# Optimization experiments

Hardware: AMD Instinct MI355X
Metric: run time of the kernel (lower is better)

The kernel has to match this reference:

```python
import jax, jax.numpy as jnp
import numpy as np

H = 512      # hidden_size
Z = 128      # z_dim
E = 512      # embedding_dim
D = 2 * H + Z  # GRU hidden / decoder state dim = 1152
V = 32000    # output_size
BS = 256
N = 128      # encoder nodes per source


def setup_inputs() -> dict:
    key = jax.random.key(0)
    ks = jax.random.split(key, 24)
    s = 0.05
    inp = {
        "prev_y": jax.random.normal(ks[0], (BS, E), jnp.float32),
        "prev_h": jax.random.normal(ks[1], (BS, D), jnp.float32),
        "equ_enc": jax.random.normal(ks[2], (BS, N, H), jnp.float32),
        "sns_enc": jax.random.normal(ks[3], (BS, N, H), jnp.float32),
        "z_sample": jax.random.normal(ks[4], (BS, Z), jnp.float32),
        "equ_mask": jax.random.randint(ks[5], (BS, N), 0, 2) > 0,
        "sns_mask": jax.random.randint(ks[6], (BS, N), 0, 2) > 0,
        # Attention (equ): W1: HxH, W2: HxD, vt: 1xH (torch Linear weight = [out,in])
        "W1e": jax.random.normal(ks[7], (H, H), jnp.float32) * s,
        "W2e": jax.random.normal(ks[8], (H, D), jnp.float32) * s,
        "vte": jax.random.normal(ks[9], (1, H), jnp.float32) * s,
        "W1s": jax.random.normal(ks[10], (H, H), jnp.float32) * s,
        "W2s": jax.random.normal(ks[11], (H, D), jnp.float32) * s,
        "vts": jax.random.normal(ks[12], (1, H), jnp.float32) * s,
        "plan_W": jax.random.normal(ks[13], (2, D), jnp.float32) * s,
        "plan_b": jax.random.normal(ks[14], (2,), jnp.float32) * s,
        "Wc": jax.random.normal(ks[15], (H, E + H), jnp.float32) * s,
        "bc": jax.random.normal(ks[16], (H,), jnp.float32) * s,
        # GRU: input H -> hidden D
        "w_ih": jax.random.normal(ks[17], (3 * D, H), jnp.float32) * s,
        "w_hh": jax.random.normal(ks[18], (3 * D, D), jnp.float32) * s,
        "b_ih": jax.random.normal(ks[19], (3 * D,), jnp.float32) * s,
        "b_hh": jax.random.normal(ks[20], (3 * D,), jnp.float32) * s,
        "Wout": jax.random.normal(ks[21], (V, D), jnp.float32) * s,
        "bout": jax.random.normal(ks[22], (V,), jnp.float32) * s,
    }
    return inp


def _attn(h, enc, mask, W1, W2, vt):
    # enc: (b,n,H), h: (b,D)
    et = jnp.einsum('bnh,kh->bnk', enc, W1)          # (b,n,H)
    dt = (h @ W2.T)[:, None, :]                       # (b,1,H)
    u = jnp.einsum('bnh,h->bn', jnp.tanh(et + dt), vt[0])
    u = jnp.where(mask, -jnp.inf, u)
    return jax.nn.softmax(u, axis=-1)                 # (b,n)


def reference(prev_y, prev_h, equ_enc, sns_enc, z_sample, equ_mask, sns_mask,
              W1e, W2e, vte, W1s, W2s, vts, plan_W, plan_b, Wc, bc,
              w_ih, w_hh, b_ih, b_hh, Wout, bout):
    aw_e = _attn(prev_h, equ_enc, equ_mask, W1e, W2e, vte)
    ctx_e = jnp.einsum('bn,bnh->bh', aw_e, equ_enc)
    aw_s = _attn(prev_h, sns_enc, sns_mask, W1s, W2s, vts)
    ctx_s = jnp.einsum('bn,bnh->bh', aw_s, sns_enc)
    plan = jax.nn.softmax(prev_h @ plan_W.T + plan_b, axis=-1)  # (b,2)
    combine = jnp.stack([ctx_e, ctx_s], axis=1)                  # (b,2,H)
    context = jnp.einsum('bk,bkh->bh', plan, combine)
    y_ctx = jnp.concatenate([prev_y, context], axis=-1)          # (b,E+H)
    x = y_ctx @ Wc.T + bc                                        # (b,H)
    # single-step GRU (torch gate order: r, z, n)
    gx = x @ w_ih.T + b_ih                                       # (b,3D)
    gh = prev_h @ w_hh.T + b_hh
    Dh = prev_h.shape[-1]
    gx_r, gx_z, gx_n = gx[:, :Dh], gx[:, Dh:2*Dh], gx[:, 2*Dh:]
    gh_r, gh_z, gh_n = gh[:, :Dh], gh[:, Dh:2*Dh], gh[:, 2*Dh:]
    r = jax.nn.sigmoid(gx_r + gh_r)
    zg = jax.nn.sigmoid(gx_z + gh_z)
    n = jnp.tanh(gx_n + r * gh_n)
    h_new = (1.0 - zg) * n + zg * prev_h                          # (b,D)
    dec_output = (h_new @ Wout.T + bout)[:, None, :]              # (b,1,V)
    dec_hidden = h_new[None]                                      # (1,b,D)
    return dec_output, dec_hidden, plan
```

## Files before the change

### kernel.cpp

```cpp
#include <hip/hip_runtime.h>
#include <stdint.h>
#include <math.h>

#define BS_  256
#define NSEQ 128
#define HH   512
#define DD   1152
#define VV   32000
#define BN_  (BS_*NSEQ)

typedef float  f32x4  __attribute__((ext_vector_type(4)));
typedef __bf16 bf16x8 __attribute__((ext_vector_type(8)));

__device__ __forceinline__ f32x4 mfma16(bf16x8 a, bf16x8 b, f32x4 c) {
    return __builtin_amdgcn_mfma_f32_16x16x32_bf16(a, b, c, 0, 0, 0);
}

__device__ __forceinline__ bf16x8 pack8(f32x4 a, f32x4 b) {
    bf16x8 v;
    v[0] = (__bf16)a[0]; v[1] = (__bf16)a[1]; v[2] = (__bf16)a[2]; v[3] = (__bf16)a[3];
    v[4] = (__bf16)b[0]; v[5] = (__bf16)b[1]; v[6] = (__bf16)b[2]; v[7] = (__bf16)b[3];
    return v;
}

__device__ __forceinline__ float tanh_fast(float x) {
    float e = __expf(2.f * x);
    return 1.f - __fdividef(2.f, e + 1.f);
}

__device__ __forceinline__ void gload16(const void* g, void* l) {
    __builtin_amdgcn_global_load_lds(
        (const __attribute__((address_space(1))) void*)g,
        (__attribute__((address_space(3))) void*)l, 16, 0, 0);
}

__global__ __launch_bounds__(256) void k_cast(const float* __restrict__ src,
                                              __bf16* __restrict__ dst, int n8)
{
    int i = blockIdx.x * 256 + threadIdx.x;
    int stride = gridDim.x * 256;
    for (; i < n8; i += stride) {
        const f32x4* s = (const f32x4*)(src + (size_t)i * 8);
        f32x4 a = s[0], b = s[1];
        *(bf16x8*)(dst + (size_t)i * 8) = pack8(a, b);
    }
}

__global__ __launch_bounds__(256) void k_attn2(
    const float* __restrict__ enc_e, const float* __restrict__ enc_s,
    const __bf16* __restrict__ W1be, const __bf16* __restrict__ W1bs,
    const float* __restrict__ vte, const float* __restrict__ vts,
    const float* __restrict__ dt_e, const float* __restrict__ dt_s,
    float* __restrict__ u_part)
{
    const int L = blockIdx.x;
    const int n = (L >> 3) & 3;
    const int G = (L & 7) + ((L >> 5) << 3);
    const int e = G >> 8;
    const int b = G & 255;

    const float*  enc = e ? enc_s : enc_e;
    const __bf16* W1  = e ? W1bs : W1be;
    const float*  vt  = e ? vts : vte;
    const float*  dt  = e ? dt_s : dt_e;

    __shared__ float  lA[2][4096];
    __shared__ __bf16 lB[2][4096];
    __shared__ float  upart[2][128];

    const int t = threadIdx.x;
    const int w = t >> 6, wr = w >> 1, wc = w & 1;
    const int lane = t & 63, g = lane >> 4, r = lane & 15;

    const float*  Ag = enc + (size_t)b * (128 * 512);
    const __bf16* Bg = W1 + (size_t)n * (128 * 512);

    int aoff[4], boff[2], aldsb[4], bldsb[2];
    #pragma unroll
    for (int i = 0; i < 4; ++i) {
        int c = i * 256 + w * 64 + lane;
        int row = c >> 3, kc = c & 7;
        aoff[i]  = row * 512 + ((kc ^ (row & 7)) << 2);
        aldsb[i] = (i * 256 + w * 64) << 2;
    }
    #pragma unroll
    for (int i = 0; i < 2; ++i) {
        int c = i * 256 + w * 64 + lane;
        int row = c >> 2, kc = c & 3;
        boff[i]  = row * 512 + ((kc ^ ((row >> 1) & 3)) << 3);
        bldsb[i] = (i * 256 + w * 64) << 3;
    }

    f32x4 acc[4][4];
    #pragma unroll
    for (int i = 0; i < 4; ++i)
        #pragma unroll
        for (int j = 0; j < 4; ++j) acc[i][j] = (f32x4){0.f, 0.f, 0.f, 0.f};

    #pragma unroll
    for (int i = 0; i < 4; ++i) gload16(Ag + aoff[i], &lA[0][aldsb[i]]);
    #pragma unroll
    for (int i = 0; i < 2; ++i) gload16(Bg + boff[i], &lB[0][bldsb[i]]);

    for (int kb = 0; kb < 16; ++kb) {
        const int buf = kb & 1;
        __syncthreads();
        if (kb + 1 < 16) {
            const int k0 = (kb + 1) * 32;
            #pragma unroll
            for (int i = 0; i < 4; ++i) gload16(Ag + aoff[i] + k0, &lA[buf ^ 1][aldsb[i]]);
            #pragma unroll
            for (int i = 0; i < 2; ++i) gload16(Bg + boff[i] + k0, &lB[buf ^ 1][bldsb[i]]);
        }
        bf16x8 af[4], bfr[4];
        #pragma unroll
        for (int j = 0; j < 4; ++j) {
            int row = wc * 64 + j * 16 + r;
            bfr[j] = *(const bf16x8*)&lB[buf][row * 32 + ((g ^ ((row >> 1) & 3)) << 3)];
        }
        #pragma unroll
        for (int i = 0; i < 4; ++i) {
            int row = wr * 64 + i * 16 + r;
            int s = row & 7;
            f32x4 a0 = *(const f32x4*)&lA[buf][row * 32 + (((g << 1) ^ s) << 2)];
            f32x4 a1 = *(const f32x4*)&lA[buf][row * 32 + ((((g << 1) | 1) ^ s) << 2)];
            af[i] = pack8(a0, a1);
        }
        #pragma unroll
        for (int i = 0; i < 4; ++i)
            #pragma unroll
            for (int j = 0; j < 4; ++j)
                acc[i][j] = mfma16(af[i], bfr[j], acc[i][j]);
    }

    float dv[4], vv[4];
    #pragma unroll
    for (int j = 0; j < 4; ++j) {
        int col = n * 128 + wc * 64 + j * 16 + r;
        dv[j] = dt[(size_t)b * 512 + col];
        vv[j] = vt[col];
    }
    #pragma unroll
    for (int i = 0; i < 4; ++i) {
        #pragma unroll
        for (int q = 0; q < 4; ++q) {
            float s = 0.f;
            #pragma unroll
            for (int j = 0; j < 4; ++j)
                s += vv[j] * tanh_fast(acc[i][j][q] + dv[j]);
            #pragma unroll
            for (int m = 1; m < 16; m <<= 1) s += __shfl_xor(s, m);
            if (r == 0) upart[wc][wr * 64 + i * 16 + g * 4 + q] = s;
        }
    }
    __syncthreads();
    if (t < 128)
        u_part[((size_t)(n * 2 + e)) * BN_ + b * 128 + t] = upart[0][t] + upart[1][t];
}

__global__ __launch_bounds__(256) void k_vocab2(
    const __bf16* __restrict__ A,
    const float* __restrict__ B,
    const float* __restrict__ bias, float* __restrict__ C)
{
    const int L = blockIdx.x;
    const int p  = (L & 7) + ((L >> 4) << 3);
    const int rr = (L >> 3) & 1;
    if (p >= 250) return;
    const int rb = rr * 128, cb = p * 128;

    __shared__ __bf16 lA[2][4096];
    __shared__ float  lB[2][4096];

    const int t = threadIdx.x;
    const int w = t >> 6, wr = w >> 1, wc = w & 1;
    const int lane = t & 63, g = lane >> 4, r = lane & 15;

    const __bf16* Ag = A + (size_t)rb * DD;
    const float*  Bg = B + (size_t)cb * DD;

    int aoff[2], boff[4], aldsb[2], bldsb[4];
    #pragma unroll
    for (int i = 0; i < 2; ++i) {
        int c = i * 256 + w * 64 + lane;
        int row = c >> 2, kc = c & 3;
        aoff[i]  = row * DD + ((kc ^ ((row >> 1) & 3)) << 3);
        aldsb[i] = (i * 256 + w * 64) << 3;
    }
    #pragma unroll
    for (int i = 0; i < 4; ++i) {
        int c = i * 256 + w * 64 + lane;
        int row = c >> 3, kc = c & 7;
        boff[i]  = row * DD + ((kc ^ (row & 7)) << 2);
        bldsb[i] = (i * 256 + w * 64) << 2;
    }

    f32x4 acc[4][4];
    #pragma unroll
    for (int i = 0; i < 4; ++i)
        #pragma unroll
        for (int j = 0; j < 4; ++j) acc[i][j] = (f32x4){0.f, 0.f, 0.f, 0.f};

    #pragma unroll
    for (int i = 0; i < 2; ++i) gload16(Ag + aoff[i], &lA[0][aldsb[i]]);
    #pragma unroll
    for (int i = 0; i < 4; ++i) gload16(Bg + boff[i], &lB[0][bldsb[i]]);

    for (int kb = 0; kb < 36; ++kb) {
        const int buf = kb & 1;
        __syncthreads();
        if (kb + 1 < 36) {
            const int k0 = (kb + 1) * 32;
            #pragma unroll
            for (int i = 0; i < 2; ++i) gload16(Ag + aoff[i] + k0, &lA[buf ^ 1][aldsb[i]]);
            #pragma unroll
            for (int i = 0; i < 4; ++i) gload16(Bg + boff[i] + k0, &lB[buf ^ 1][bldsb[i]]);
        }
        bf16x8 af[4], bfr[4];
        #pragma unroll
        for (int i = 0; i < 4; ++i) {
            int row = wr * 64 + i * 16 + r;
            af[i] = *(const bf16x8*)&lA[buf][row * 32 + ((g ^ ((row >> 1) & 3)) << 3)];
        }
        #pragma unroll
        for (int j = 0; j < 4; ++j) {
            int row = wc * 64 + j * 16 + r;
            int s = row & 7;
            f32x4 b0 = *(const f32x4*)&lB[buf][row * 32 + (((g << 1) ^ s) << 2)];
            f32x4 b1 = *(const f32x4*)&lB[buf][row * 32 + ((((g << 1) | 1) ^ s) << 2)];
            bfr[j] = pack8(b0, b1);
        }
        #pragma unroll
        for (int i = 0; i < 4; ++i)
            #pragma unroll
            for (int j = 0; j < 4; ++j)
                acc[i][j] = mfma16(af[i], bfr[j], acc[i][j]);
    }

    #pragma unroll
    for (int j = 0; j < 4; ++j) {
        const int col = cb + wc * 64 + j * 16 + r;
        const float bv = bias[col];
        #pragma unroll
        for (int i = 0; i < 4; ++i) {
            #pragma unroll
            for (int q = 0; q < 4; ++q) {
                const int row = rb + wr * 64 + i * 16 + g * 4 + q;
                C[(size_t)row * VV + col] = acc[i][j][q] + bv;
            }
        }
    }
}

__global__ __launch_bounds__(256) void k_tile128(
    const float* __restrict__ A, const float* __restrict__ B,
    const float* __restrict__ bias, float* __restrict__ C,
    int K, int ldc)
{
    const int rb = blockIdx.x * 128;
    const int cb = blockIdx.y * 128;
    const int t = threadIdx.x;
    const int w = t >> 6, wr = w >> 1, wc = w & 1;
    const int lane = t & 63, g = lane >> 4, r = lane & 15;
    const int s_row = t >> 1, s_h = t & 1;

    __shared__ bf16x8 sm[2][2][512];

    const float* Ap = A + (size_t)(rb + s_row) * K + s_h * 16;
    const float* Bp = B + (size_t)(cb + s_row) * K + s_h * 16;

    const int kg0 = 2 * s_h, kg1 = 2 * s_h + 1;
    const int swz0 = kg0 * 128 + ((s_row & 112) | ((s_row ^ (kg0 << 2)) & 15));
    const int swz1 = kg1 * 128 + ((s_row & 112) | ((s_row ^ (kg1 << 2)) & 15));

    int ai[4], bi[4];
    #pragma unroll
    for (int i = 0; i < 4; ++i) {
        ai[i] = g * 128 + wr * 64 + i * 16 + ((r ^ (g << 2)) & 15);
        bi[i] = g * 128 + wc * 64 + i * 16 + ((r ^ (g << 2)) & 15);
    }

    const int KS = K >> 5;
    f32x4 pa0 = ((const f32x4*)Ap)[0], pa1 = ((const f32x4*)Ap)[1],
          pa2 = ((const f32x4*)Ap)[2], pa3 = ((const f32x4*)Ap)[3];
    f32x4 pb0 = ((const f32x4*)Bp)[0], pb1 = ((const f32x4*)Bp)[1],
          pb2 = ((const f32x4*)Bp)[2], pb3 = ((const f32x4*)Bp)[3];

    f32x4 acc[4][4];
    #pragma unroll
    for (int i = 0; i < 4; ++i)
        #pragma unroll
        for (int j = 0; j < 4; ++j) acc[i][j] = (f32x4){0.f, 0.f, 0.f, 0.f};

    for (int kb = 0; kb < KS; ++kb) {
        const int buf = kb & 1;
        sm[buf][0][swz0] = pack8(pa0, pa1);
        sm[buf][0][swz1] = pack8(pa2, pa3);
        sm[buf][1][swz0] = pack8(pb0, pb1);
        sm[buf][1][swz1] = pack8(pb2, pb3);
        __syncthreads();
        if (kb + 1 < KS) {
            const float* a2 = Ap + (kb + 1) * 32;
            const float* b2 = Bp + (kb + 1) * 32;
            pa0 = ((const f32x4*)a2)[0]; pa1 = ((const f32x4*)a2)[1];
            pa2 = ((const f32x4*)a2)[2]; pa3 = ((const f32x4*)a2)[3];
            pb0 = ((const f32x4*)b2)[0]; pb1 = ((const f32x4*)b2)[1];
            pb2 = ((const f32x4*)b2)[2]; pb3 = ((const f32x4*)b2)[3];
        }
        bf16x8 af[4], bfr[4];
        #pragma unroll
        for (int i = 0; i < 4; ++i) af[i]  = sm[buf][0][ai[i]];
        #pragma unroll
        for (int j = 0; j < 4; ++j) bfr[j] = sm[buf][1][bi[j]];
        #pragma unroll
        for (int i = 0; i < 4; ++i)
            #pragma unroll
            for (int j = 0; j < 4; ++j)
                acc[i][j] = mfma16(af[i], bfr[j], acc[i][j]);
    }

    #pragma unroll
    for (int j = 0; j < 4; ++j) {
        const int col = cb + wc * 64 + j * 16 + r;
        const float bv = bias ? bias[col] : 0.f;
        #pragma unroll
        for (int i = 0; i < 4; ++i) {
            #pragma unroll
            for (int q = 0; q < 4; ++q) {
                const int row = rb + wr * 64 + i * 16 + g * 4 + q;
                C[(size_t)row * ldc + col] = acc[i][j][q] + bv;
            }
        }
    }
}

__global__ __launch_bounds__(256) void k_prevh(
    const float* __restrict__ prev_h, const float* __restrict__ W2e,
    const float* __restrict__ W2s, const float* __restrict__ w_hh,
    const float* __restrict__ b_hh,
    float* __restrict__ dt_e, float* __restrict__ dt_s, float* __restrict__ gh)
{
    const int cb = blockIdx.x * 64;
    const int rb = blockIdx.y * 64;
    const int t  = threadIdx.x;
    const int w = t >> 6, lane = t & 63, g = lane >> 4, r = lane & 15;
    const int s_row = t >> 2, s_kc = t & 3;
    const int K = DD;

    __shared__ bf16x8 sm[2][2][256];

    const float* Ap = prev_h + (size_t)(rb + s_row) * K + s_kc * 8;
    const float* Bp;
    {
        int brow = cb + s_row;
        if (cb < 512)        Bp = W2e + (size_t)brow * K;
        else if (cb < 1024)  Bp = W2s + (size_t)(brow - 512) * K;
        else                 Bp = w_hh + (size_t)(brow - 1024) * K;
        Bp += s_kc * 8;
    }

    const int KS = K >> 5;
    f32x4 pa0 = *(const f32x4*)Ap, pa1 = *(const f32x4*)(Ap + 4);
    f32x4 pb0 = *(const f32x4*)Bp, pb1 = *(const f32x4*)(Bp + 4);

    f32x4 acc[4] = {{0,0,0,0},{0,0,0,0},{0,0,0,0},{0,0,0,0}};

    for (int kb = 0; kb < KS; ++kb) {
        sm[kb & 1][0][s_kc * 64 + s_row] = pack8(pa0, pa1);
        sm[kb & 1][1][s_kc * 64 + s_row] = pack8(pb0, pb1);
        __syncthreads();
        if (kb + 1 < KS) {
            const float* a2 = Ap + (kb + 1) * 32;
            const float* b2 = Bp + (kb + 1) * 32;
            pa0 = *(const f32x4*)a2; pa1 = *(const f32x4*)(a2 + 4);
            pb0 = *(const f32x4*)b2; pb1 = *(const f32x4*)(b2 + 4);
        }
        bf16x8 af = sm[kb & 1][0][g * 64 + w * 16 + r];
        #pragma unroll
        for (int j = 0; j < 4; ++j) {
            bf16x8 bf = sm[kb & 1][1][g * 64 + j * 16 + r];
            acc[j] = mfma16(af, bf, acc[j]);
        }
    }

    #pragma unroll
    for (int j = 0; j < 4; ++j) {
        int col = cb + j * 16 + r;
        #pragma unroll
        for (int q = 0; q < 4; ++q) {
            int row = rb + w * 16 + g * 4 + q;
            float v = acc[j][q];
            if (cb < 512)       dt_e[(size_t)row * 512 + col] = v;
            else if (cb < 1024) dt_s[(size_t)row * 512 + (col - 512)] = v;
            else {
                int c0 = col - 1024;
                gh[(size_t)row * 3456 + c0] = v + b_hh[c0];
            }
        }
    }
}

__global__ __launch_bounds__(256) void k_ctx(
    const float* __restrict__ u_part, const int* __restrict__ mask_e,
    const int* __restrict__ mask_s, const float* __restrict__ enc_e,
    const float* __restrict__ enc_s, const float* __restrict__ prev_h,
    const float* __restrict__ plan_W, const float* __restrict__ plan_b,
    const float* __restrict__ prev_y,
    float* __restrict__ y_ctx, float* __restrict__ plan_out)
{
    const int b = blockIdx.x;
    const int rh = blockIdx.y;
    const int t = threadIdx.x;
    const int lane = t & 63, wid = t >> 6, half = t >> 7, n = t & 127;

    __shared__ float aw[2][128];
    __shared__ float red[16];
    __shared__ float planv[2];

    const int* mask = half ? mask_s : mask_e;
    float uv = u_part[(size_t)(0 * 2 + half) * BN_ + b * 128 + n]
             + u_part[(size_t)(1 * 2 + half) * BN_ + b * 128 + n]
             + u_part[(size_t)(2 * 2 + half) * BN_ + b * 128 + n]
             + u_part[(size_t)(3 * 2 + half) * BN_ + b * 128 + n];
    bool msk = mask[b * 128 + n] != 0;
    float val = msk ? -3.4e38f : uv;

    float mx = val;
    #pragma unroll
    for (int m = 1; m < 64; m <<= 1) mx = fmaxf(mx, __shfl_xor(mx, m));
    if (lane == 0) red[wid] = mx;
    __syncthreads();
    mx = fmaxf(red[half * 2], red[half * 2 + 1]);
    float ex = msk ? 0.f : __expf(uv - mx);
    float sm = ex;
    #pragma unroll
    for (int m = 1; m < 64; m <<= 1) sm += __shfl_xor(sm, m);
    if (lane == 0) red[4 + wid] = sm;
    __syncthreads();
    sm = red[4 + half * 2] + red[4 + half * 2 + 1];
    aw[half][n] = ex / sm;

    float p0 = 0.f, p1 = 0.f;
    for (int i = t; i < DD; i += 256) {
        float hv = prev_h[(size_t)b * DD + i];
        p0 += hv * plan_W[i];
        p1 += hv * plan_W[DD + i];
    }
    #pragma unroll
    for (int m = 1; m < 64; m <<= 1) { p0 += __shfl_xor(p0, m); p1 += __shfl_xor(p1, m); }
    if (lane == 0) { red[8 + wid] = p0; red[12 + wid] = p1; }
    __syncthreads();
    if (t == 0) {
        float l0 = red[8] + red[9] + red[10] + red[11] + plan_b[0];
        float l1 = red[12] + red[13] + red[14] + red[15] + plan_b[1];
        float mm = fmaxf(l0, l1);
        float e0 = __expf(l0 - mm), e1 = __expf(l1 - mm);
        float ss = e0 + e1;
        planv[0] = e0 / ss; planv[1] = e1 / ss;
        if (rh == 0) {
            plan_out[b * 2 + 0] = planv[0];
            plan_out[b * 2 + 1] = planv[1];
        }
    }
    __syncthreads();

    const int ee = t >> 7;
    const int tt = t & 127;
    const float pl = planv[ee];
    const float* base = (ee ? enc_s : enc_e) + (size_t)b * 65536 + (size_t)(rh * 64) * 512 + tt * 4;
    f32x4 accv = {0.f, 0.f, 0.f, 0.f};
    #pragma unroll 4
    for (int row = 0; row < 64; ++row) {
        f32x4 v = *(const f32x4*)(base + (size_t)row * 512);
        float a = aw[ee][rh * 64 + row];
        accv += a * v;
    }
    float* dst = y_ctx + (size_t)b * 1024 + 512 + tt * 4;
    atomicAdd(dst + 0, pl * accv[0]);
    atomicAdd(dst + 1, pl * accv[1]);
    atomicAdd(dst + 2, pl * accv[2]);
    atomicAdd(dst + 3, pl * accv[3]);

    if (rh == 0 && t < 128) {
        f32x4 v = *(const f32x4*)(prev_y + (size_t)b * 512 + t * 4);
        *(f32x4*)(y_ctx + (size_t)b * 1024 + t * 4) = v;
    }
}

__global__ __launch_bounds__(256) void k_gemm_bias(
    const float* __restrict__ A, const float* __restrict__ B,
    const float* __restrict__ bias, float* __restrict__ C,
    int K, int ldc)
{
    const int cb = blockIdx.x * 64;
    const int rb = blockIdx.y * 64;
    const int t  = threadIdx.x;
    const int w = t >> 6, lane = t & 63, g = lane >> 4, r = lane & 15;
    const int s_row = t >> 2, s_kc = t & 3;

    __shared__ bf16x8 sm[2][2][256];

    const float* Ap = A + (size_t)(rb + s_row) * K + s_kc * 8;
    const float* Bp = B + (size_t)(cb + s_row) * K + s_kc * 8;

    const int KS = K >> 5;
    f32x4 pa0 = *(const f32x4*)Ap, pa1 = *(const f32x4*)(Ap + 4);
    f32x4 pb0 = *(const f32x4*)Bp, pb1 = *(const f32x4*)(Bp + 4);

    f32x4 acc[4] = {{0,0,0,0},{0,0,0,0},{0,0,0,0},{0,0,0,0}};

    for (int kb = 0; kb < KS; ++kb) {
        sm[kb & 1][0][s_kc * 64 + s_row] = pack8(pa0, pa1);
        sm[kb & 1][1][s_kc * 64 + s_row] = pack8(pb0, pb1);
        __syncthreads();
        if (kb + 1 < KS) {
            const float* a2 = Ap + (kb + 1) * 32;
            const float* b2 = Bp + (kb + 1) * 32;
            pa0 = *(const f32x4*)a2; pa1 = *(const f32x4*)(a2 + 4);
            pb0 = *(const f32x4*)b2; pb1 = *(const f32x4*)(b2 + 4);
        }
        bf16x8 af = sm[kb & 1][0][g * 64 + w * 16 + r];
        #pragma unroll
        for (int j = 0; j < 4; ++j) {
            bf16x8 bf = sm[kb & 1][1][g * 64 + j * 16 + r];
            acc[j] = mfma16(af, bf, acc[j]);
        }
    }
    #pragma unroll
    for (int j = 0; j < 4; ++j) {
        int col = cb + j * 16 + r;
        float bv = bias ? bias[col] : 0.f;
        #pragma unroll
        for (int q = 0; q < 4; ++q) {
            int row = rb + w * 16 + g * 4 + q;
            C[(size_t)row * ldc + col] = acc[j][q] + bv;
        }
    }
}

__global__ __launch_bounds__(384) void k_gru(
    const float* __restrict__ gx, const float* __restrict__ gh,
    const float* __restrict__ prev_h, float* __restrict__ h_new,
    float* __restrict__ out_hidden, __bf16* __restrict__ h_new_bf)
{
    int d = blockIdx.x * 384 + threadIdx.x;
    int b = blockIdx.y;
    size_t o3 = (size_t)b * 3456;
    float xr = gx[o3 + d], xz = gx[o3 + 1152 + d], xn = gx[o3 + 2304 + d];
    float hr = gh[o3 + d], hz = gh[o3 + 1152 + d], hn = gh[o3 + 2304 + d];
    float rr = 1.f / (1.f + __expf(-(xr + hr)));
    float zz = 1.f / (1.f + __expf(-(xz + hz)));
    float nv = tanhf(xn + rr * hn);
    float hv = (1.f - zz) * nv + zz * prev_h[(size_t)b * DD + d];
    h_new[(size_t)b * DD + d] = hv;
    out_hidden[(size_t)b * DD + d] = hv;
    h_new_bf[(size_t)b * DD + d] = (__bf16)hv;
}

extern "C" void kernel_launch(void* const* d_in, const int* in_sizes, int n_in,
                              void* d_out, int out_size, void* d_ws, size_t ws_size,
                              hipStream_t stream)
{
    const float* prev_y = (const float*)d_in[0];
    const float* prev_h = (const float*)d_in[1];
    const float* enc_e  = (const float*)d_in[2];
    const float* enc_s  = (const float*)d_in[3];
    const int*   mask_e = (const int*)d_in[5];
    const int*   mask_s = (const int*)d_in[6];
    const float* W1e    = (const float*)d_in[7];
    const float* W2e    = (const float*)d_in[8];
    const float* vte    = (const float*)d_in[9];
    const float* W1s    = (const float*)d_in[10];
    const float* W2s    = (const float*)d_in[11];
    const float* vts    = (const float*)d_in[12];
    const float* plan_W = (const float*)d_in[13];
    const float* plan_b = (const float*)d_in[14];
    const float* Wc     = (const float*)d_in[15];
    const float* bc     = (const float*)d_in[16];
    const float* w_ih   = (const float*)d_in[17];
    const float* w_hh   = (const float*)d_in[18];
    const float* b_ih   = (const float*)d_in[19];
    const float* b_hh   = (const float*)d_in[20];
    const float* Wout   = (const float*)d_in[21];
    const float* bout   = (const float*)d_in[22];

    float* out = (float*)d_out;
    float* ws  = (float*)d_ws;

    float* gh     = ws;
    float* big2   = ws + 884736;
    float* upxx   = big2 + 884736;
    float* y_ctx  = upxx + 262144;
    float* h_new  = y_ctx + 262144;
    __bf16* W1be  = (__bf16*)(h_new + 294912);
    __bf16* W1bs  = W1be + 262144;
    __bf16* hnbf  = W1bs + 262144;

    float* dt_e  = big2;
    float* dt_s  = big2 + 131072;
    float* gx    = big2;
    float* u_part = upxx;
    float* xx    = upxx;

    float* dec_out  = out;
    float* dec_hid  = out + 8192000;
    float* plan_out = out + 8486912;

    hipMemsetAsync(y_ctx, 0, 262144 * sizeof(float), stream);

    k_cast<<<dim3(128), 256, 0, stream>>>(W1e, W1be, 32768);
    k_cast<<<dim3(128), 256, 0, stream>>>(W1s, W1bs, 32768);

    k_prevh<<<dim3(70, 4), 256, 0, stream>>>(prev_h, W2e, W2s, w_hh, b_hh,
                                             dt_e, dt_s, gh);

    k_attn2<<<dim3(2048), 256, 0, stream>>>(
        enc_e, enc_s, W1be, W1bs, vte, vts, dt_e, dt_s, u_part);

    k_ctx<<<dim3(BS_, 2), 256, 0, stream>>>(u_part, mask_e, mask_s, enc_e, enc_s,
                                            prev_h, plan_W, plan_b, prev_y,
                                            y_ctx, plan_out);

    k_gemm_bias<<<dim3(8, 4), 256, 0, stream>>>(y_ctx, Wc, bc, xx, 1024, 512);
    k_tile128<<<dim3(2, 27), 256, 0, stream>>>(xx, w_ih, b_ih, gx, 512, 3456);

    k_gru<<<dim3(3, BS_), 384, 0, stream>>>(gx, gh, prev_h, h_new, dec_hid, hnbf);

    k_vocab2<<<dim3(512), 256, 0, stream>>>(hnbf, Wout, bout, dec_out);
}
```

Measured before the change: 579.4 us.

## Fuse attention scoring, softmax and context into one kernel with LDS-resident encoder

Each block now loads one batch row's encoder tile once into shared memory as bf16. It computes scores across all W1 output columns, then the masked softmax and the weighted context sum, all from that resident tile. This removes the repeated fp32 encoder reads from global memory and the separate context kernel. The plan softmax moves to its own small kernel. The trade-off is lower occupancy from the large LDS footprint, plus a context sum computed from bf16-rounded encoder values.

Measured after the change: 582.2 us. About the same (+0.5%).

```diff
diff --git a/kernel.cpp b/kernel.cpp
--- a/kernel.cpp
+++ b/kernel.cpp
@@ -46,116 +46,200 @@
     }
 }
 
-__global__ __launch_bounds__(256) void k_attn2(
+__global__ __launch_bounds__(128) void k_plan(
+    const float* __restrict__ prev_h, const float* __restrict__ plan_W,
+    const float* __restrict__ plan_b, const float* __restrict__ prev_y,
+    float* __restrict__ y_ctx, float* __restrict__ plan_out)
+{
+    const int b = blockIdx.x;
+    const int t = threadIdx.x;
+    const int lane = t & 63, w = t >> 6;
+    __shared__ float red[4];
+
+    float p0 = 0.f, p1 = 0.f;
+    for (int i = t; i < DD; i += 128) {
+        float hv = prev_h[(size_t)b * DD + i];
+        p0 += hv * plan_W[i];
+        p1 += hv * plan_W[DD + i];
+    }
+    #pragma unroll
+    for (int m = 1; m < 64; m <<= 1) { p0 += __shfl_xor(p0, m); p1 += __shfl_xor(p1, m); }
+    if (lane == 0) { red[w] = p0; red[2 + w] = p1; }
+    __syncthreads();
+    if (t == 0) {
+        float l0 = red[0] + red[1] + plan_b[0];
+        float l1 = red[2] + red[3] + plan_b[1];
+        float mm = fmaxf(l0, l1);
+        float e0 = __expf(l0 - mm), e1 = __expf(l1 - mm);
+        float ss = e0 + e1;
+        plan_out[b * 2 + 0] = e0 / ss;
+        plan_out[b * 2 + 1] = e1 / ss;
+    }
+    f32x4 v = *(const f32x4*)(prev_y + (size_t)b * 512 + t * 4);
+    *(f32x4*)(y_ctx + (size_t)b * 1024 + t * 4) = v;
+}
+
+__global__ __launch_bounds__(512, 1) void k_attn3(
     const float* __restrict__ enc_e, const float* __restrict__ enc_s,
     const __bf16* __restrict__ W1be, const __bf16* __restrict__ W1bs,
     const float* __restrict__ vte, const float* __restrict__ vts,
     const float* __restrict__ dt_e, const float* __restrict__ dt_s,
-    float* __restrict__ u_part)
+    const int* __restrict__ mask_e, const int* __restrict__ mask_s,
+    const float* __restrict__ plan_out,
+    float* __restrict__ y_ctx)
 {
     const int L = blockIdx.x;
-    const int n = (L >> 3) & 3;
-    const int G = (L & 7) + ((L >> 5) << 3);
-    const int e = G >> 8;
-    const int b = G & 255;
-
-    const float*  enc = e ? enc_s : enc_e;
-    const __bf16* W1  = e ? W1bs : W1be;
-    const float*  vt  = e ? vts : vte;
-    const float*  dt  = e ? dt_s : dt_e;
-
-    __shared__ float  lA[2][4096];
-    __shared__ __bf16 lB[2][4096];
-    __shared__ float  upart[2][128];
+    const int e = L & 1;
+    const int b = L >> 1;
+
+    const float*  enc  = e ? enc_s : enc_e;
+    const __bf16* W1   = e ? W1bs : W1be;
+    const float*  vt   = e ? vts : vte;
+    const float*  dt   = e ? dt_s : dt_e;
+    const int*    mask = e ? mask_s : mask_e;
+
+    __shared__ __bf16 Asm[128 * 512];
+    __shared__ __bf16 Bsm[2][4096];
+    __shared__ float  u_acc[128];
+    __shared__ float  red[4];
+    __shared__ float  ctxp[2][512];
 
     const int t = threadIdx.x;
-    const int w = t >> 6, wr = w >> 1, wc = w & 1;
+    const int w = t >> 6, wr = w >> 2, wcq = w & 3;
     const int lane = t & 63, g = lane >> 4, r = lane & 15;
 
-    const float*  Ag = enc + (size_t)b * (128 * 512);
-    const __bf16* Bg = W1 + (size_t)n * (128 * 512);
-
-    int aoff[4], boff[2], aldsb[4], bldsb[2];
-    #pragma unroll
-    for (int i = 0; i < 4; ++i) {
-        int c = i * 256 + w * 64 + lane;
-        int row = c >> 3, kc = c & 7;
-        aoff[i]  = row * 512 + ((kc ^ (row & 7)) << 2);
-        aldsb[i] = (i * 256 + w * 64) << 2;
-    }
-    #pragma unroll
-    for (int i = 0; i < 2; ++i) {
-        int c = i * 256 + w * 64 + lane;
-        int row = c >> 2, kc = c & 3;
-        boff[i]  = row * 512 + ((kc ^ ((row >> 1) & 3)) << 3);
-        bldsb[i] = (i * 256 + w * 64) << 3;
-    }
-
-    f32x4 acc[4][4];
-    #pragma unroll
-    for (int i = 0; i < 4; ++i)
-        #pragma unroll
-        for (int j = 0; j < 4; ++j) acc[i][j] = (f32x4){0.f, 0.f, 0.f, 0.f};
-
-    #pragma unroll
-    for (int i = 0; i < 4; ++i) gload16(Ag + aoff[i], &lA[0][aldsb[i]]);
-    #pragma unroll
-    for (int i = 0; i < 2; ++i) gload16(Bg + boff[i], &lB[0][bldsb[i]]);
-
-    for (int kb = 0; kb < 16; ++kb) {
-        const int buf = kb & 1;
+    if (t < 128) u_acc[t] = 0.f;
+
+    {
+        const float* Ag = enc + (size_t)b * (128 * 512);
+        #pragma unroll
+        for (int i = 0; i < 16; ++i) {
+            int u = t + i * 512;
+            int row = u >> 6, cc = u & 63;
+            const f32x4* src = (const f32x4*)(Ag + row * 512 + cc * 8);
+            f32x4 a0 = src[0], a1 = src[1];
+            *(bf16x8*)&Asm[row * 512 + ((cc ^ (row & 7)) << 3)] = pack8(a0, a1);
+        }
+    }
+
+    const int q_row = t >> 2, q_c = t & 3;
+    const int q_cc  = q_c ^ ((q_row >> 1) & 3);
+    const __bf16* Bsrc0 = W1 + q_row * 512 + q_cc * 8;
+    const int BdstE = w * 512;
+
+    gload16(Bsrc0, &Bsm[0][BdstE]);
+
+    f32x4 acc[4][2];
+    float dv[2], vv[2];
+
+    for (int ks = 0; ks < 64; ++ks) {
+        const int ph = ks >> 4, kb = ks & 15;
+        const int buf = ks & 1;
         __syncthreads();
-        if (kb + 1 < 16) {
-            const int k0 = (kb + 1) * 32;
-            #pragma unroll
-            for (int i = 0; i < 4; ++i) gload16(Ag + aoff[i] + k0, &lA[buf ^ 1][aldsb[i]]);
-            #pragma unroll
-            for (int i = 0; i < 2; ++i) gload16(Bg + boff[i] + k0, &lB[buf ^ 1][bldsb[i]]);
-        }
-        bf16x8 af[4], bfr[4];
-        #pragma unroll
-        for (int j = 0; j < 4; ++j) {
-            int row = wc * 64 + j * 16 + r;
-            bfr[j] = *(const bf16x8*)&lB[buf][row * 32 + ((g ^ ((row >> 1) & 3)) << 3)];
+        if (ks + 1 < 64) {
+            const int ph_n = (ks + 1) >> 4, kb_n = (ks + 1) & 15;
+            gload16(Bsrc0 + ph_n * 65536 + kb_n * 32, &Bsm[buf ^ 1][BdstE]);
+        }
+        if (kb == 0) {
+            #pragma unroll
+            for (int i = 0; i < 4; ++i)
+                #pragma unroll
+                for (int j = 0; j < 2; ++j) acc[i][j] = (f32x4){0.f, 0.f, 0.f, 0.f};
+            #pragma unroll
+            for (int j = 0; j < 2; ++j) {
+                int col = ph * 128 + wcq * 32 + j * 16 + r;
+                dv[j] = dt[(size_t)b * 512 + col];
+                vv[j] = vt[col];
+            }
+        }
+        bf16x8 af[4], bfr[2];
+        #pragma unroll
+        for (int j = 0; j < 2; ++j) {
+            int nb = wcq * 32 + j * 16 + r;
+            bfr[j] = *(const bf16x8*)&Bsm[buf][nb * 32 + ((g ^ ((nb >> 1) & 3)) << 3)];
         }
         #pragma unroll
         for (int i = 0; i < 4; ++i) {
-            int row = wr * 64 + i * 16 + r;
-            int s = row & 7;
-            f32x4 a0 = *(const f32x4*)&lA[buf][row * 32 + (((g << 1) ^ s) << 2)];
-            f32x4 a1 = *(const f32x4*)&lA[buf][row * 32 + ((((g << 1) | 1) ^ s) << 2)];
-            af[i] = pack8(a0, a1);
+            int ra = wr * 64 + i * 16 + r;
+            af[i] = *(const bf16x8*)&Asm[ra * 512 + (((kb * 4 + g) ^ (ra & 7)) << 3)];
         }
         #pragma unroll
         for (int i = 0; i < 4; ++i)
             #pragma unroll
-            for (int j = 0; j < 4; ++j)
+            for (int j = 0; j < 2; ++j)
                 acc[i][j] = mfma16(af[i], bfr[j], acc[i][j]);
-    }
-
-    float dv[4], vv[4];
-    #pragma unroll
-    for (int j = 0; j < 4; ++j) {
-        int col = n * 128 + wc * 64 + j * 16 + r;
-        dv[j] = dt[(size_t)b * 512 + col];
-        vv[j] = vt[col];
-    }
-    #pragma unroll
-    for (int i = 0; i < 4; ++i) {
-        #pragma unroll
-        for (int q = 0; q < 4; ++q) {
-            float s = 0.f;
-            #pragma unroll
-            for (int j = 0; j < 4; ++j)
-                s += vv[j] * tanh_fast(acc[i][j][q] + dv[j]);
-            #pragma unroll
-            for (int m = 1; m < 16; m <<= 1) s += __shfl_xor(s, m);
-            if (r == 0) upart[wc][wr * 64 + i * 16 + g * 4 + q] = s;
-        }
-    }
+
+        if (kb == 15) {
+            #pragma unroll
+            for (int i = 0; i < 4; ++i) {
+                #pragma unroll
+                for (int q = 0; q < 4; ++q) {
+                    float s = vv[0] * tanh_fast(acc[i][0][q] + dv[0])
+                            + vv[1] * tanh_fast(acc[i][1][q] + dv[1]);
+                    #pragma unroll
+                    for (int m = 1; m < 16; m <<= 1) s += __shfl_xor(s, m);
+                    if (r == 0)
+                        atomicAdd(&u_acc[wr * 64 + i * 16 + g * 4 + q], s);
+                }
+            }
+        }
+    }
+
     __syncthreads();
-    if (t < 128)
-        u_part[((size_t)(n * 2 + e)) * BN_ + b * 128 + t] = upart[0][t] + upart[1][t];
+
+    float exv = 0.f;
+    if (t < 128) {
+        float uv = u_acc[t];
+        bool msk = mask[b * 128 + t] != 0;
+        float val = msk ? -3.4e38f : uv;
+        float mx = val;
+        #pragma unroll
+        for (int m = 1; m < 64; m <<= 1) mx = fmaxf(mx, __shfl_xor(mx, m));
+        if (lane == 0) red[w] = mx;
+        exv = msk ? 0.f : uv;
+    }
+    __syncthreads();
+    float smv = 0.f;
+    if (t < 128) {
+        float mx = fmaxf(red[0], red[1]);
+        bool msk = mask[b * 128 + t] != 0;
+        exv = msk ? 0.f : __expf(exv - mx);
+        smv = exv;
+        #pragma unroll
+        for (int m = 1; m < 64; m <<= 1) smv += __shfl_xor(smv, m);
+        if (lane == 0) red[2 + w] = smv;
+    }
+    __syncthreads();
+    if (t < 128) {
+        u_acc[t] = exv / (red[2] + red[3]);
+    }
+    __syncthreads();
+
+    if (t < 128) {
+        int cc = t & 63, rh = t >> 6;
+        f32x4 s0 = {0.f, 0.f, 0.f, 0.f}, s1 = {0.f, 0.f, 0.f, 0.f};
+        for (int row = rh * 64; row < rh * 64 + 64; ++row) {
+            bf16x8 v = *(const bf16x8*)&Asm[row * 512 + ((cc ^ (row & 7)) << 3)];
+            float a = u_acc[row];
+            s0[0] += a * (float)v[0]; s0[1] += a * (float)v[1];
+            s0[2] += a * (float)v[2]; s0[3] += a * (float)v[3];
+            s1[0] += a * (float)v[4]; s1[1] += a * (float)v[5];
+            s1[2] += a * (float)v[6]; s1[3] += a * (float)v[7];
+        }
+        *(f32x4*)&ctxp[rh][cc * 8]     = s0;
+        *(f32x4*)&ctxp[rh][cc * 8 + 4] = s1;
+    }
+    __syncthreads();
+    if (t < 128) {
+        float pl = plan_out[b * 2 + e];
+        f32x4 c0 = *(const f32x4*)&ctxp[0][t * 4];
+        f32x4 c1 = *(const f32x4*)&ctxp[1][t * 4];
+        float* dst = y_ctx + (size_t)b * 1024 + 512 + t * 4;
+        atomicAdd(dst + 0, pl * (c0[0] + c1[0]));
+        atomicAdd(dst + 1, pl * (c0[1] + c1[1]));
+        atomicAdd(dst + 2, pl * (c0[2] + c1[2]));
+        atomicAdd(dst + 3, pl * (c0[3] + c1[3]));
+    }
 }
 
 __global__ __launch_bounds__(256) void k_vocab2(
@@ -397,93 +481,6 @@
                 gh[(size_t)row * 3456 + c0] = v + b_hh[c0];
             }
         }
-    }
-}
-
-__global__ __launch_bounds__(256) void k_ctx(
-    const float* __restrict__ u_part, const int* __restrict__ mask_e,
-    const int* __restrict__ mask_s, const float* __restrict__ enc_e,
-    const float* __restrict__ enc_s, const float* __restrict__ prev_h,
-    const float* __restrict__ plan_W, const float* __restrict__ plan_b,
-    const float* __restrict__ prev_y,
-    float* __restrict__ y_ctx, float* __restrict__ plan_out)
-{
-    const int b = blockIdx.x;
-    const int rh = blockIdx.y;
-    const int t = threadIdx.x;
-    const int lane = t & 63, wid = t >> 6, half = t >> 7, n = t & 127;
-
-    __shared__ float aw[2][128];
-    __shared__ float red[16];
-    __shared__ float planv[2];
-
-    const int* mask = half ? mask_s : mask_e;
-    float uv = u_part[(size_t)(0 * 2 + half) * BN_ + b * 128 + n]
-             + u_part[(size_t)(1 * 2 + half) * BN_ + b * 128 + n]
-             + u_part[(size_t)(2 * 2 + half) * BN_ + b * 128 + n]
-             + u_part[(size_t)(3 * 2 + half) * BN_ + b * 128 + n];
-    bool msk = mask[b * 128 + n] != 0;
-    float val = msk ? -3.4e38f : uv;
-
-    float mx = val;
-    #pragma unroll
-    for (int m = 1; m < 64; m <<= 1) mx = fmaxf(mx, __shfl_xor(mx, m));
-    if (lane == 0) red[wid] = mx;
-    __syncthreads();
-    mx = fmaxf(red[half * 2], red[half * 2 + 1]);
-    float ex = msk ? 0.f : __expf(uv - mx);
-    float sm = ex;
-    #pragma unroll
-    for (int m = 1; m < 64; m <<= 1) sm += __shfl_xor(sm, m);
-    if (lane == 0) red[4 + wid] = sm;
-    __syncthreads();
-    sm = red[4 + half * 2] + red[4 + half * 2 + 1];
-    aw[half][n] = ex / sm;
-
-    float p0 = 0.f, p1 = 0.f;
-    for (int i = t; i < DD; i += 256) {
-        float hv = prev_h[(size_t)b * DD + i];
-        p0 += hv * plan_W[i];
-        p1 += hv * plan_W[DD + i];
-    }
-    #pragma unroll
-    for (int m = 1; m < 64; m <<= 1) { p0 += __shfl_xor(p0, m); p1 += __shfl_xor(p1, m); }
-    if (lane == 0) { red[8 + wid] = p0; red[12 + wid] = p1; }
-    __syncthreads();
-    if (t == 0) {
-        float l0 = red[8] + red[9] + red[10] + red[11] + plan_b[0];
-        float l1 = red[12] + red[13] + red[14] + red[15] + plan_b[1];
-        float mm = fmaxf(l0, l1);
-        float e0 = __expf(l0 - mm), e1 = __expf(l1 - mm);
-        float ss = e0 + e1;
-        planv[0] = e0 / ss; planv[1] = e1 / ss;
-        if (rh == 0) {
-            plan_out[b * 2 + 0] = planv[0];
-            plan_out[b * 2 + 1] = planv[1];
-        }
-    }
-    __syncthreads();
-
-    const int ee = t >> 7;
-    const int tt = t & 127;
-    const float pl = planv[ee];
-    const float* base = (ee ? enc_s : enc_e) + (size_t)b * 65536 + (size_t)(rh * 64) * 512 + tt * 4;
-    f32x4 accv = {0.f, 0.f, 0.f, 0.f};
-    #pragma unroll 4
-    for (int row = 0; row < 64; ++row) {
-        f32x4 v = *(const f32x4*)(base + (size_t)row * 512);
-        float a = aw[ee][rh * 64 + row];
-        accv += a * v;
-    }
-    float* dst = y_ctx + (size_t)b * 1024 + 512 + tt * 4;
-    atomicAdd(dst + 0, pl * accv[0]);
-    atomicAdd(dst + 1, pl * accv[1]);
-    atomicAdd(dst + 2, pl * accv[2]);
-    atomicAdd(dst + 3, pl * accv[3]);
-
-    if (rh == 0 && t < 128) {
-        f32x4 v = *(const f32x4*)(prev_y + (size_t)b * 512 + t * 4);
-        *(f32x4*)(y_ctx + (size_t)b * 1024 + t * 4) = v;
     }
 }
 
@@ -599,7 +596,6 @@
     float* dt_e  = big2;
     float* dt_s  = big2 + 131072;
     float* gx    = big2;
-    float* u_part = upxx;
     float* xx    = upxx;
 
     float* dec_out  = out;
@@ -611,15 +607,15 @@
     k_cast<<<dim3(128), 256, 0, stream>>>(W1e, W1be, 32768);
     k_cast<<<dim3(128), 256, 0, stream>>>(W1s, W1bs, 32768);
 
+    k_plan<<<dim3(BS_), 128, 0, stream>>>(prev_h, plan_W, plan_b, prev_y,
+                                          y_ctx, plan_out);
+
     k_prevh<<<dim3(70, 4), 256, 0, stream>>>(prev_h, W2e, W2s, w_hh, b_hh,
                                              dt_e, dt_s, gh);
 
-    k_attn2<<<dim3(2048), 256, 0, stream>>>(
-        enc_e, enc_s, W1be, W1bs, vte, vts, dt_e, dt_s, u_part);
-
-    k_ctx<<<dim3(BS_, 2), 256, 0, stream>>>(u_part, mask_e, mask_s, enc_e, enc_s,
-                                            prev_h, plan_W, plan_b, prev_y,
-                                            y_ctx, plan_out);
+    k_attn3<<<dim3(512), 512, 0, stream>>>(
+        enc_e, enc_s, W1be, W1bs, vte, vts, dt_e, dt_s,
+        mask_e, mask_s, plan_out, y_ctx);
 
     k_gemm_bias<<<dim3(8, 4), 256, 0, stream>>>(y_ctx, Wc, bc, xx, 1024, 512);
     k_tile128<<<dim3(2, 27), 256, 0, stream>>>(xx, w_ih, b_ih, gx, 512, 3456);
```
